# Kernel tuning notes

Hardware: AMD Instinct MI355X
Metric: run time of the kernel (lower is better)

The kernel has to match this reference:

```python
import jax, jax.numpy as jnp
import numpy as np

EMBED_DIM = 768
NUM_HEADS = 12
HEAD_DIM = EMBED_DIM // NUM_HEADS
SCALING = HEAD_DIM ** -0.5
B, S = 2, 2048


def setup_inputs() -> dict:
    key = jax.random.key(0)
    k1, k2, k3 = jax.random.split(key, 3)
    x_q = jax.random.normal(k1, (B, S, EMBED_DIM), dtype=jnp.float32)
    # xavier-uniform-ish scaling for weights
    lim_qkv = (6.0 / (EMBED_DIM + 3 * EMBED_DIM)) ** 0.5
    lim_out = (6.0 / (2 * EMBED_DIM)) ** 0.5
    w_qkv = jax.random.uniform(k2, (3 * EMBED_DIM, EMBED_DIM), jnp.float32, -lim_qkv, lim_qkv)
    b_qkv = jnp.zeros((3 * EMBED_DIM,), jnp.float32)
    w_out = jax.random.uniform(k3, (EMBED_DIM, EMBED_DIM), jnp.float32, -lim_out, lim_out)
    b_out = jnp.zeros((EMBED_DIM,), jnp.float32)
    return {"x_q": x_q, "w_qkv": w_qkv, "b_qkv": b_qkv, "w_out": w_out, "b_out": b_out}


def reference(x_q, w_qkv, b_qkv, w_out, b_out):
    b_sz, s_len, _ = x_q.shape
    # qkv projection: (B,S,3E) -> (B,S,3,H,hd) -> split
    qkv = x_q @ w_qkv.T + b_qkv
    qkv = qkv.reshape(b_sz, s_len, 3, NUM_HEADS, HEAD_DIM)
    q = qkv[:, :, 0].transpose(0, 2, 1, 3) * SCALING  # (B,H,S,hd)
    k = qkv[:, :, 1].transpose(0, 2, 1, 3)
    v = qkv[:, :, 2].transpose(0, 2, 1, 3)
    attn = jnp.einsum("bhsd,bhtd->bhst", q, k)  # (B,H,S,S)
    attn = jax.nn.softmax(attn.astype(jnp.float32), axis=-1).astype(attn.dtype)
    out = jnp.einsum("bhst,bhtd->bhsd", attn, v)  # (B,H,S,hd)
    out = out.transpose(0, 2, 1, 3).reshape(b_sz, s_len, EMBED_DIM)
    return out @ w_out.T + b_out
```

## Files before the change

### kernel.cpp

```cpp
#include <hip/hip_runtime.h>
#include <hip/hip_bf16.h>
#include <math.h>

typedef unsigned short u16;
typedef unsigned int u32;
typedef __attribute__((ext_vector_type(8))) short bf16x8;
typedef __attribute__((ext_vector_type(4))) short bf16x4;
typedef __attribute__((ext_vector_type(4))) float f32x4;

#define EMBED 768
#define NHEADS 12
#define HDIM 64
#define NBATCH 2
#define SEQ 2048
#define NTOK 4096
#define QKV_N 2304
#define BHTOT 24
#define QSCALE 0.18033688011112042f

__device__ __forceinline__ u16 f2b(float f) {
    __hip_bfloat16 h = __float2bfloat16(f);
    return __builtin_bit_cast(u16, h);
}
__device__ __forceinline__ u32 pk2(float a, float b) {
    return (u32)f2b(a) | ((u32)f2b(b) << 16);
}
__device__ __forceinline__ f32x4 mfma32(bf16x8 a, bf16x8 b, f32x4 c) {
    return __builtin_amdgcn_mfma_f32_16x16x32_bf16(a, b, c, 0, 0, 0);
}
#if __has_builtin(__builtin_amdgcn_mfma_f32_16x16x16_bf16)
__device__ __forceinline__ f32x4 mfma16(bf16x4 a, bf16x4 b, f32x4 c) {
    return __builtin_amdgcn_mfma_f32_16x16x16_bf16(a, b, c, 0, 0, 0);
}
#else
__device__ __forceinline__ f32x4 mfma16(bf16x4 a, bf16x4 b, f32x4 c) {
    return __builtin_amdgcn_mfma_f32_16x16x16bf16_1k(a, b, c, 0, 0, 0);
}
#endif

__device__ __forceinline__ float exp2_hw(float x) {
#if __has_builtin(__builtin_amdgcn_exp2f)
    return __builtin_amdgcn_exp2f(x);
#else
    float r;
    asm("v_exp_f32 %0, %1" : "=v"(r) : "v"(x));
    return r;
#endif
}

__device__ __forceinline__ void async16(const u16* g, u16* l) {
    __builtin_amdgcn_global_load_lds(
        (const __attribute__((address_space(1))) unsigned int*)g,
        (__attribute__((address_space(3))) unsigned int*)l,
        16, 0, 0);
}

__global__ __launch_bounds__(256)
void cast_kernel(const float* __restrict__ s0, u16* __restrict__ d0, int n0,
                 const float* __restrict__ s1, u16* __restrict__ d1, int n1,
                 const float* __restrict__ s2, u16* __restrict__ d2, int n2)
{
    int idx = (blockIdx.x * 256 + threadIdx.x) * 4;
    const float* s; u16* d; int i;
    if (idx < n0)            { s = s0; d = d0; i = idx; }
    else if (idx < n0 + n1)  { s = s1; d = d1; i = idx - n0; }
    else                     { s = s2; d = d2; i = idx - n0 - n1; if (i >= n2) return; }
    float4 v = *(const float4*)&s[i];
    ushort4 o;
    o.x = f2b(v.x); o.y = f2b(v.y); o.z = f2b(v.z); o.w = f2b(v.w);
    *(ushort4*)&d[i] = o;
}

__global__ __launch_bounds__(256, 4)
void qkv_gemm(const u16* __restrict__ A, const u16* __restrict__ W,
              const float* __restrict__ bias,
              u16* __restrict__ Qb, u16* __restrict__ Kb, u16* __restrict__ VT)
{
    __shared__ __align__(16) u16 smem[18432];
    u16* As = smem;
    u16* Bs = smem + 8192;
    const int m0 = blockIdx.x * 128;
    const int n0 = blockIdx.y * 128;
    const int tid = threadIdx.x;
    const int w = tid >> 6, l = tid & 63;
    const int c = l & 15, q = l >> 4;
    const int wm = (w >> 1) * 64, wn = (w & 1) * 64;
    const int sr = l >> 2;
    const int gch2 = (l & 3) ^ ((l >> 3) & 3);

    #pragma unroll
    for (int j = 0; j < 2; ++j) {
        int row = j * 64 + w * 16 + sr;
        int seg = (j * 64 + w * 16) * 32;
        async16(&A[(size_t)(m0 + row) * EMBED + gch2 * 8], &As[seg + l * 8]);
        async16(&W[(size_t)(n0 + row) * EMBED + gch2 * 8], &Bs[seg + l * 8]);
    }

    f32x4 acc[4][4] = {};
    const int NK = EMBED / 32;

    #pragma unroll 2
    for (int kt = 0; kt < NK; ++kt) {
        const int cur = kt & 1;
        __syncthreads();
        if (kt + 1 < NK) {
            int k0 = (kt + 1) * 32;
            #pragma unroll
            for (int j = 0; j < 2; ++j) {
                int row = j * 64 + w * 16 + sr;
                int seg = (cur ^ 1) * 4096 + (j * 64 + w * 16) * 32;
                async16(&A[(size_t)(m0 + row) * EMBED + k0 + gch2 * 8], &As[seg + l * 8]);
                async16(&W[(size_t)(n0 + row) * EMBED + k0 + gch2 * 8], &Bs[seg + l * 8]);
            }
        }
        const u16* Ab = As + cur * 4096;
        const u16* Bb = Bs + cur * 4096;
        const int cs = (q ^ ((c >> 1) & 3)) << 3;
        bf16x8 af[4], bfr[4];
        #pragma unroll
        for (int i = 0; i < 4; ++i)
            af[i] = *(const bf16x8*)&Ab[(wm + i * 16 + c) * 32 + cs];
        #pragma unroll
        for (int j = 0; j < 4; ++j)
            bfr[j] = *(const bf16x8*)&Bb[(wn + j * 16 + c) * 32 + cs];
        #pragma unroll
        for (int i = 0; i < 4; ++i)
            #pragma unroll
            for (int j = 0; j < 4; ++j)
                acc[i][j] = mfma32(af[i], bfr[j], acc[i][j]);
    }

    const int p = n0 / EMBED;
    const int ncol0 = n0 + wn;
    const int h = (ncol0 % EMBED) / HDIM;
    const int mrow0 = m0 + wm;
    const int b = mrow0 >> 11;
    const int s0 = mrow0 & (SEQ - 1);

    if (p < 2) {
        u16* dst = (p == 0) ? Qb : Kb;
        const float mul = (p == 0) ? QSCALE : 1.0f;
        #pragma unroll
        for (int j = 0; j < 4; ++j) {
            int n = ncol0 + j * 16 + c;
            int d = j * 16 + c;
            float bval = bias[n];
            #pragma unroll
            for (int i = 0; i < 4; ++i) {
                #pragma unroll
                for (int r = 0; r < 4; ++r) {
                    int s = s0 + i * 16 + q * 4 + r;
                    float v = (acc[i][j][r] + bval) * mul;
                    dst[(((size_t)(b * NHEADS + h)) * SEQ + s) * HDIM + d] = f2b(v);
                }
            }
        }
    } else {
        __syncthreads();
        u16* T = smem + w * (64 * 72);
        #pragma unroll
        for (int j = 0; j < 4; ++j) {
            int n = ncol0 + j * 16 + c;
            float bval = bias[n];
            #pragma unroll
            for (int i = 0; i < 4; ++i) {
                uint2 pr;
                pr.x = pk2(acc[i][j][0] + bval, acc[i][j][1] + bval);
                pr.y = pk2(acc[i][j][2] + bval, acc[i][j][3] + bval);
                *(uint2*)&T[(j * 16 + c) * 72 + i * 16 + q * 4] = pr;
            }
        }
        const size_t vtbase = ((size_t)(b * NHEADS + h)) * HDIM * SEQ + s0;
        #pragma unroll
        for (int ii = 0; ii < 8; ++ii) {
            int d = (l >> 3) + 8 * ii;
            int sch = (l & 7) * 8;
            uint4 vv = *(const uint4*)&T[d * 72 + sch];
            *(uint4*)&VT[vtbase + (size_t)d * SEQ + sch] = vv;
        }
    }
}

__global__ __launch_bounds__(256, 3)
void attn_kernel(const u16* __restrict__ Qb, const u16* __restrict__ Kb,
                 const u16* __restrict__ VT, u16* __restrict__ AO)
{
    __shared__ __align__(16) u16 Ks[3][4096];
    __shared__ __align__(16) u16 Vs[3][4096];

    const int blk = blockIdx.x;
    const int g = blk & 7, kk = blk >> 3;
    const int bh = g * 3 + (kk >> 5);
    const int qt = kk & 31;

    const int tid = threadIdx.x;
    const int w = tid >> 6, l = tid & 63;
    const int c = l & 15, q = l >> 4;
    const int wq = w >> 1, wk = w & 1;

    const u16* qg = Qb + ((size_t)bh * SEQ + qt * 64 + wq * 32) * HDIM;
    const u16* kg = Kb + ((size_t)bh * SEQ) * HDIM;
    const u16* vg = VT + ((size_t)bh * HDIM) * SEQ;

    const int r8 = l >> 3, ch = l & 7;
    const int gch = ch ^ r8;

    bf16x8 bq[2][2];
    #pragma unroll
    for (int qb2 = 0; qb2 < 2; ++qb2) {
        bq[qb2][0] = *(const bf16x8*)&qg[(qb2 * 16 + c) * HDIM + q * 8];
        bq[qb2][1] = *(const bf16x8*)&qg[(qb2 * 16 + c) * HDIM + 32 + q * 8];
    }

    f32x4 o[4][2] = {};
    float lrow[2] = {0.f, 0.f};

    const int NT = SEQ / 64;

#define STAGE(JT, BS) {                                                       \
    int row0 = w * 16 + r8;                                                   \
    async16(&kg[(size_t)((JT) * 64 + row0) * HDIM + gch * 8],                 \
            &Ks[BS][(w * 16) * 64 + l * 8]);                                  \
    async16(&vg[(size_t)row0 * SEQ + (JT) * 64 + gch * 8],                    \
            &Vs[BS][(w * 16) * 64 + l * 8]);                                  \
    async16(&kg[(size_t)((JT) * 64 + row0 + 8) * HDIM + gch * 8],             \
            &Ks[BS][(w * 16 + 8) * 64 + l * 8]);                              \
    async16(&vg[(size_t)(row0 + 8) * SEQ + (JT) * 64 + gch * 8],              \
            &Vs[BS][(w * 16 + 8) * 64 + l * 8]);                              \
}

#define QKT(SN, BN) {                                                         \
    __builtin_amdgcn_s_setprio(1);                                            \
    _Pragma("unroll")                                                         \
    for (int kb2 = 0; kb2 < 2; ++kb2) {                                       \
        bf16x8 ak0 = *(const bf16x8*)&Ks[BN][(wk * 32 + kb2 * 16 + c) * 64 +  \
                                             (((q    ) ^ (c & 7)) << 3)];     \
        bf16x8 ak1 = *(const bf16x8*)&Ks[BN][(wk * 32 + kb2 * 16 + c) * 64 +  \
                                             (((q | 4) ^ (c & 7)) << 3)];     \
        _Pragma("unroll")                                                     \
        for (int qb2 = 0; qb2 < 2; ++qb2) {                                   \
            f32x4 zz = {};                                                    \
            zz = mfma32(ak0, bq[qb2][0], zz);                                 \
            SN[kb2][qb2] = mfma32(ak1, bq[qb2][1], zz);                       \
        }                                                                     \
    }                                                                         \
    __builtin_amdgcn_s_setprio(0);                                            \
}

#define SOFTPV(SC, BC) {                                                      \
    _Pragma("unroll")                                                         \
    for (int kb2 = 0; kb2 < 2; ++kb2)                                         \
        _Pragma("unroll")                                                     \
        for (int qb2 = 0; qb2 < 2; ++qb2) {                                   \
            float p0 = exp2_hw(SC[kb2][qb2][0]);                              \
            float p1 = exp2_hw(SC[kb2][qb2][1]);                              \
            float p2 = exp2_hw(SC[kb2][qb2][2]);                              \
            float p3 = exp2_hw(SC[kb2][qb2][3]);                              \
            SC[kb2][qb2][0] = p0; SC[kb2][qb2][1] = p1;                       \
            SC[kb2][qb2][2] = p2; SC[kb2][qb2][3] = p3;                       \
            lrow[qb2] += (p0 + p1) + (p2 + p3);                               \
        }                                                                     \
    bf16x4 bp[2][2];                                                          \
    _Pragma("unroll")                                                         \
    for (int kb2 = 0; kb2 < 2; ++kb2)                                         \
        _Pragma("unroll")                                                     \
        for (int qb2 = 0; qb2 < 2; ++qb2) {                                   \
            uint2 pr;                                                         \
            pr.x = pk2(SC[kb2][qb2][0], SC[kb2][qb2][1]);                     \
            pr.y = pk2(SC[kb2][qb2][2], SC[kb2][qb2][3]);                     \
            bp[kb2][qb2] = __builtin_bit_cast(bf16x4, pr);                    \
        }                                                                     \
    __builtin_amdgcn_s_setprio(1);                                            \
    _Pragma("unroll")                                                         \
    for (int db = 0; db < 4; ++db) {                                          \
        bf16x4 av0 = *(const bf16x4*)&Vs[BC][(db * 16 + c) * 64 +             \
                  (((4 * wk     + (q >> 1)) ^ (c & 7)) << 3) + ((q & 1) << 2)]; \
        bf16x4 av1 = *(const bf16x4*)&Vs[BC][(db * 16 + c) * 64 +             \
                  (((4 * wk + 2 + (q >> 1)) ^ (c & 7)) << 3) + ((q & 1) << 2)]; \
        _Pragma("unroll")                                                     \
        for (int qb2 = 0; qb2 < 2; ++qb2) {                                   \
            o[db][qb2] = mfma16(av0, bp[0][qb2], o[db][qb2]);                 \
            o[db][qb2] = mfma16(av1, bp[1][qb2], o[db][qb2]);                 \
        }                                                                     \
    }                                                                         \
    __builtin_amdgcn_s_setprio(0);                                            \
}

#define BODY(J, SC, SN, BC, BN, BS) {                                         \
    asm volatile("s_waitcnt vmcnt(0)" ::: "memory");                          \
    __builtin_amdgcn_s_barrier();                                             \
    if ((J) + 2 < NT) STAGE((J) + 2, BS);                                     \
    if ((J) + 1 < NT) QKT(SN, BN);                                            \
    SOFTPV(SC, BC);                                                           \
}

    f32x4 scA[2][2], scB[2][2];

    STAGE(0, 0);
    STAGE(1, 1);
    asm volatile("s_waitcnt vmcnt(4)" ::: "memory");
    __builtin_amdgcn_s_barrier();
    QKT(scA, 0);

    for (int jb = 0; jb < 30; jb += 6) {
        BODY(jb + 0, scA, scB, 0, 1, 2);
        BODY(jb + 1, scB, scA, 1, 2, 0);
        BODY(jb + 2, scA, scB, 2, 0, 1);
        BODY(jb + 3, scB, scA, 0, 1, 2);
        BODY(jb + 4, scA, scB, 1, 2, 0);
        BODY(jb + 5, scB, scA, 2, 0, 1);
    }
    BODY(30, scA, scB, 0, 1, 2);
    SOFTPV(scB, 1);

#undef STAGE
#undef QKT
#undef SOFTPV
#undef BODY

    #pragma unroll
    for (int qb2 = 0; qb2 < 2; ++qb2) {
        lrow[qb2] += __shfl_xor(lrow[qb2], 16);
        lrow[qb2] += __shfl_xor(lrow[qb2], 32);
    }

    __syncthreads();
    float* SCR = (float*)&Ks[0][0];
    float* LR  = SCR + 4096;

    if (wk == 1) {
        #pragma unroll
        for (int db = 0; db < 4; ++db)
            #pragma unroll
            for (int qb2 = 0; qb2 < 2; ++qb2)
                *(f32x4*)&SCR[((wq * 8 + db * 2 + qb2) << 8) + l * 4] = o[db][qb2];
        if (q == 0) {
            LR[(wq * 2 + 0) * 16 + c] = lrow[0];
            LR[(wq * 2 + 1) * 16 + c] = lrow[1];
        }
    }
    __syncthreads();

    if (wk == 0) {
        float inv[2];
        #pragma unroll
        for (int qb2 = 0; qb2 < 2; ++qb2)
            inv[qb2] = 1.0f / (lrow[qb2] + LR[(wq * 2 + qb2) * 16 + c]);
        const int b = bh / NHEADS, h = bh % NHEADS;
        #pragma unroll
        for (int qb2 = 0; qb2 < 2; ++qb2) {
            const int s = qt * 64 + wq * 32 + qb2 * 16 + c;
            u16* ao = AO + ((size_t)(b * SEQ + s)) * EMBED + h * HDIM;
            #pragma unroll
            for (int db = 0; db < 4; ++db) {
                f32x4 part = *(const f32x4*)&SCR[((wq * 8 + db * 2 + qb2) << 8) + l * 4];
                f32x4 t = o[db][qb2] + part;
                uint2 oo;
                oo.x = pk2(t[0] * inv[qb2], t[1] * inv[qb2]);
                oo.y = pk2(t[2] * inv[qb2], t[3] * inv[qb2]);
                *(uint2*)&ao[db * 16 + q * 4] = oo;
            }
        }
    }
}

__global__ __launch_bounds__(256)
void out_gemm(const u16* __restrict__ A, const u16* __restrict__ W,
              const float* __restrict__ bias, float* __restrict__ out)
{
    __shared__ __align__(16) u16 As[2][2048];
    __shared__ __align__(16) u16 Bs[2][2048];
    const int m0 = blockIdx.x * 64;
    const int n0 = blockIdx.y * 64;
    const int tid = threadIdx.x;
    const int w = tid >> 6, l = tid & 63;
    const int c = l & 15, q = l >> 4;
    const int sr = l >> 2;
    const int gch2 = (l & 3) ^ ((l >> 3) & 3);

    {
        int row = w * 16 + sr;
        async16(&A[(size_t)(m0 + row) * EMBED + gch2 * 8], &As[0][(w * 16) * 32 + l * 8]);
        async16(&W[(size_t)(n0 + row) * EMBED + gch2 * 8], &Bs[0][(w * 16) * 32 + l * 8]);
    }

    f32x4 acc[4] = {};
    const int NK = EMBED / 32;

    #pragma unroll 2
    for (int kt = 0; kt < NK; ++kt) {
        const int cur = kt & 1;
        __syncthreads();
        if (kt + 1 < NK) {
            int k0 = (kt + 1) * 32;
            int row = w * 16 + sr;
            async16(&A[(size_t)(m0 + row) * EMBED + k0 + gch2 * 8],
                    &As[cur ^ 1][(w * 16) * 32 + l * 8]);
            async16(&W[(size_t)(n0 + row) * EMBED + k0 + gch2 * 8],
                    &Bs[cur ^ 1][(w * 16) * 32 + l * 8]);
        }
        const int cs = (q ^ ((c >> 1) & 3)) << 3;
        bf16x8 af = *(const bf16x8*)&As[cur][(w * 16 + c) * 32 + cs];
        bf16x8 bfr[4];
        #pragma unroll
        for (int j = 0; j < 4; ++j)
            bfr[j] = *(const bf16x8*)&Bs[cur][(j * 16 + c) * 32 + cs];
        #pragma unroll
        for (int j = 0; j < 4; ++j)
            acc[j] = mfma32(af, bfr[j], acc[j]);
    }

    #pragma unroll
    for (int j = 0; j < 4; ++j) {
        int n = n0 + j * 16 + c;
        float bval = bias[n];
        #pragma unroll
        for (int r = 0; r < 4; ++r) {
            int m = m0 + w * 16 + q * 4 + r;
            out[(size_t)m * EMBED + n] = acc[j][r] + bval;
        }
    }
}

extern "C" void kernel_launch(void* const* d_in, const int* in_sizes, int n_in,
                              void* d_out, int out_size, void* d_ws, size_t ws_size,
                              hipStream_t stream)
{
    const float* x    = (const float*)d_in[0];
    const float* wqkv = (const float*)d_in[1];
    const float* bqkv = (const float*)d_in[2];
    const float* wout = (const float*)d_in[3];
    const float* bout = (const float*)d_in[4];
    float* out = (float*)d_out;

    const int nx  = NTOK * EMBED;
    const int nwq = QKV_N * EMBED;
    const int nwo = EMBED * EMBED;
    const size_t per = (size_t)NBATCH * NHEADS * SEQ * HDIM;

    u16* xb    = (u16*)d_ws;
    u16* wqkvb = xb + nx;
    u16* woutb = wqkvb + nwq;
    u16* Qb    = woutb + nwo;
    u16* Kb    = Qb + per;
    u16* VT    = Kb + per;
    u16* AO    = VT + per;

    int castTot = (nx + nwq + nwo) / 4;
    cast_kernel<<<castTot / 256, 256, 0, stream>>>(x, xb, nx, wqkv, wqkvb, nwq, wout, woutb, nwo);

    dim3 g1(NTOK / 128, QKV_N / 128);
    qkv_gemm<<<g1, 256, 0, stream>>>(xb, wqkvb, bqkv, Qb, Kb, VT);

    attn_kernel<<<BHTOT * 32, 256, 0, stream>>>(Qb, Kb, VT, AO);

    dim3 g3(NTOK / 64, EMBED / 64);
    out_gemm<<<g3, 256, 0, stream>>>(AO, woutb, bout, out);
}
```

Baseline: 149.9 us.

## Use three-stage async-copy pipeline in QKV and output projection GEMMs

Both projection GEMMs move from double buffering to a triple-buffered LDS ring, issuing loads two k-tiles ahead. Each step waits with an explicit vmcnt count instead of a full __syncthreads drain, and the MFMA block runs at raised wave priority. This hides more global-load latency behind compute, but uses more LDS per block, and the qkv kernel's occupancy hint drops from 4 to 3 blocks. NK=24 divides by 3, so the unrolled loop stays exact.

```diff
diff --git a/kernel.cpp b/kernel.cpp
--- a/kernel.cpp
+++ b/kernel.cpp
@@ -71,14 +71,12 @@
     *(ushort4*)&d[i] = o;
 }
 
-__global__ __launch_bounds__(256, 4)
+__global__ __launch_bounds__(256, 3)
 void qkv_gemm(const u16* __restrict__ A, const u16* __restrict__ W,
               const float* __restrict__ bias,
               u16* __restrict__ Qb, u16* __restrict__ Kb, u16* __restrict__ VT)
 {
-    __shared__ __align__(16) u16 smem[18432];
-    u16* As = smem;
-    u16* Bs = smem + 8192;
+    __shared__ __align__(16) u16 smem[24576];
     const int m0 = blockIdx.x * 128;
     const int n0 = blockIdx.y * 128;
     const int tid = threadIdx.x;
@@ -87,48 +85,57 @@
     const int wm = (w >> 1) * 64, wn = (w & 1) * 64;
     const int sr = l >> 2;
     const int gch2 = (l & 3) ^ ((l >> 3) & 3);
-
-    #pragma unroll
-    for (int j = 0; j < 2; ++j) {
-        int row = j * 64 + w * 16 + sr;
-        int seg = (j * 64 + w * 16) * 32;
-        async16(&A[(size_t)(m0 + row) * EMBED + gch2 * 8], &As[seg + l * 8]);
-        async16(&W[(size_t)(n0 + row) * EMBED + gch2 * 8], &Bs[seg + l * 8]);
-    }
+    const int NK = EMBED / 32;
+
+#define QSTAGE(KT, BS) {                                                      \
+    int k0 = (KT) * 32;                                                       \
+    _Pragma("unroll")                                                         \
+    for (int j = 0; j < 2; ++j) {                                             \
+        int row = j * 64 + w * 16 + sr;                                       \
+        int seg = (BS) * 8192 + (j * 64 + w * 16) * 32;                       \
+        async16(&A[(size_t)(m0 + row) * EMBED + k0 + gch2 * 8],               \
+                &smem[seg + l * 8]);                                          \
+        async16(&W[(size_t)(n0 + row) * EMBED + k0 + gch2 * 8],               \
+                &smem[seg + 4096 + l * 8]);                                   \
+    }                                                                         \
+}
 
     f32x4 acc[4][4] = {};
-    const int NK = EMBED / 32;
-
-    #pragma unroll 2
-    for (int kt = 0; kt < NK; ++kt) {
-        const int cur = kt & 1;
-        __syncthreads();
-        if (kt + 1 < NK) {
-            int k0 = (kt + 1) * 32;
-            #pragma unroll
-            for (int j = 0; j < 2; ++j) {
-                int row = j * 64 + w * 16 + sr;
-                int seg = (cur ^ 1) * 4096 + (j * 64 + w * 16) * 32;
-                async16(&A[(size_t)(m0 + row) * EMBED + k0 + gch2 * 8], &As[seg + l * 8]);
-                async16(&W[(size_t)(n0 + row) * EMBED + k0 + gch2 * 8], &Bs[seg + l * 8]);
-            }
-        }
-        const u16* Ab = As + cur * 4096;
-        const u16* Bb = Bs + cur * 4096;
-        const int cs = (q ^ ((c >> 1) & 3)) << 3;
-        bf16x8 af[4], bfr[4];
-        #pragma unroll
-        for (int i = 0; i < 4; ++i)
-            af[i] = *(const bf16x8*)&Ab[(wm + i * 16 + c) * 32 + cs];
-        #pragma unroll
-        for (int j = 0; j < 4; ++j)
-            bfr[j] = *(const bf16x8*)&Bb[(wn + j * 16 + c) * 32 + cs];
-        #pragma unroll
-        for (int i = 0; i < 4; ++i)
-            #pragma unroll
-            for (int j = 0; j < 4; ++j)
-                acc[i][j] = mfma32(af[i], bfr[j], acc[i][j]);
-    }
+
+#define QBODY(KT, BC, BS) {                                                   \
+    if ((KT) + 1 < NK) asm volatile("s_waitcnt vmcnt(4)" ::: "memory");       \
+    else               asm volatile("s_waitcnt vmcnt(0)" ::: "memory");       \
+    __builtin_amdgcn_s_barrier();                                             \
+    if ((KT) + 2 < NK) QSTAGE((KT) + 2, BS);                                  \
+    const u16* Ab = &smem[(BC) * 8192];                                       \
+    const u16* Bb = &smem[(BC) * 8192 + 4096];                                \
+    const int cs = (q ^ ((c >> 1) & 3)) << 3;                                 \
+    bf16x8 af[4], bfr[4];                                                     \
+    _Pragma("unroll")                                                         \
+    for (int i = 0; i < 4; ++i)                                               \
+        af[i] = *(const bf16x8*)&Ab[(wm + i * 16 + c) * 32 + cs];             \
+    _Pragma("unroll")                                                         \
+    for (int j = 0; j < 4; ++j)                                               \
+        bfr[j] = *(const bf16x8*)&Bb[(wn + j * 16 + c) * 32 + cs];            \
+    __builtin_amdgcn_s_setprio(1);                                            \
+    _Pragma("unroll")                                                         \
+    for (int i = 0; i < 4; ++i)                                               \
+        _Pragma("unroll")                                                     \
+        for (int j = 0; j < 4; ++j)                                           \
+            acc[i][j] = mfma32(af[i], bfr[j], acc[i][j]);                     \
+    __builtin_amdgcn_s_setprio(0);                                            \
+}
+
+    QSTAGE(0, 0);
+    QSTAGE(1, 1);
+
+    for (int kt0 = 0; kt0 < NK; kt0 += 3) {
+        QBODY(kt0 + 0, 0, 2);
+        QBODY(kt0 + 1, 1, 0);
+        QBODY(kt0 + 2, 2, 1);
+    }
+#undef QSTAGE
+#undef QBODY
 
     const int p = n0 / EMBED;
     const int ncol0 = n0 + wn;
@@ -364,12 +371,11 @@
     }
 }
 
-__global__ __launch_bounds__(256)
+__global__ __launch_bounds__(256, 3)
 void out_gemm(const u16* __restrict__ A, const u16* __restrict__ W,
               const float* __restrict__ bias, float* __restrict__ out)
 {
-    __shared__ __align__(16) u16 As[2][2048];
-    __shared__ __align__(16) u16 Bs[2][2048];
+    __shared__ __align__(16) u16 smem[12288];
     const int m0 = blockIdx.x * 64;
     const int n0 = blockIdx.y * 64;
     const int tid = threadIdx.x;
@@ -377,38 +383,50 @@
     const int c = l & 15, q = l >> 4;
     const int sr = l >> 2;
     const int gch2 = (l & 3) ^ ((l >> 3) & 3);
-
-    {
-        int row = w * 16 + sr;
-        async16(&A[(size_t)(m0 + row) * EMBED + gch2 * 8], &As[0][(w * 16) * 32 + l * 8]);
-        async16(&W[(size_t)(n0 + row) * EMBED + gch2 * 8], &Bs[0][(w * 16) * 32 + l * 8]);
-    }
+    const int NK = EMBED / 32;
+
+#define OSTAGE(KT, BS) {                                                      \
+    int k0 = (KT) * 32;                                                       \
+    int row = w * 16 + sr;                                                    \
+    int seg = (BS) * 4096 + (w * 16) * 32;                                    \
+    async16(&A[(size_t)(m0 + row) * EMBED + k0 + gch2 * 8],                   \
+            &smem[seg + l * 8]);                                              \
+    async16(&W[(size_t)(n0 + row) * EMBED + k0 + gch2 * 8],                   \
+            &smem[seg + 2048 + l * 8]);                                       \
+}
 
     f32x4 acc[4] = {};
-    const int NK = EMBED / 32;
-
-    #pragma unroll 2
-    for (int kt = 0; kt < NK; ++kt) {
-        const int cur = kt & 1;
-        __syncthreads();
-        if (kt + 1 < NK) {
-            int k0 = (kt + 1) * 32;
-            int row = w * 16 + sr;
-            async16(&A[(size_t)(m0 + row) * EMBED + k0 + gch2 * 8],
-                    &As[cur ^ 1][(w * 16) * 32 + l * 8]);
-            async16(&W[(size_t)(n0 + row) * EMBED + k0 + gch2 * 8],
-                    &Bs[cur ^ 1][(w * 16) * 32 + l * 8]);
-        }
-        const int cs = (q ^ ((c >> 1) & 3)) << 3;
-        bf16x8 af = *(const bf16x8*)&As[cur][(w * 16 + c) * 32 + cs];
-        bf16x8 bfr[4];
-        #pragma unroll
-        for (int j = 0; j < 4; ++j)
-            bfr[j] = *(const bf16x8*)&Bs[cur][(j * 16 + c) * 32 + cs];
-        #pragma unroll
-        for (int j = 0; j < 4; ++j)
-            acc[j] = mfma32(af, bfr[j], acc[j]);
-    }
+
+#define OBODY(KT, BC, BS) {                                                   \
+    if ((KT) + 1 < NK) asm volatile("s_waitcnt vmcnt(2)" ::: "memory");       \
+    else               asm volatile("s_waitcnt vmcnt(0)" ::: "memory");       \
+    __builtin_amdgcn_s_barrier();                                             \
+    if ((KT) + 2 < NK) OSTAGE((KT) + 2, BS);                                  \
+    const u16* Ab = &smem[(BC) * 4096];                                       \
+    const u16* Bb = &smem[(BC) * 4096 + 2048];                                \
+    const int cs = (q ^ ((c >> 1) & 3)) << 3;                                 \
+    bf16x8 af = *(const bf16x8*)&Ab[(w * 16 + c) * 32 + cs];                  \
+    bf16x8 bfr[4];                                                            \
+    _Pragma("unroll")                                                         \
+    for (int j = 0; j < 4; ++j)                                               \
+        bfr[j] = *(const bf16x8*)&Bb[(j * 16 + c) * 32 + cs];                 \
+    __builtin_amdgcn_s_setprio(1);                                            \
+    _Pragma("unroll")                                                         \
+    for (int j = 0; j < 4; ++j)                                               \
+        acc[j] = mfma32(af, bfr[j], acc[j]);                                  \
+    __builtin_amdgcn_s_setprio(0);                                            \
+}
+
+    OSTAGE(0, 0);
+    OSTAGE(1, 1);
+
+    for (int kt0 = 0; kt0 < NK; kt0 += 3) {
+        OBODY(kt0 + 0, 0, 2);
+        OBODY(kt0 + 1, 1, 0);
+        OBODY(kt0 + 2, 2, 1);
+    }
+#undef OSTAGE
+#undef OBODY
 
     #pragma unroll
     for (int j = 0; j < 4; ++j) {
```

Result: no change. 150.9 us (+0.7%).
